# Performance work log

Measured on AMD Instinct MI355X. Metric: run time of the kernel, lower is better.

The kernel has to match this reference:

```python
import jax, jax.numpy as jnp
import numpy as np

B, N, F_IN, S, F_OUT = 16, 128, 8, 8, 64
KN_HID = 32  # kernel_network=[32]
FC_HID = 32


def setup_inputs() -> dict:
    key = jax.random.key(0)
    ks = jax.random.split(key, 13)
    # sparse-ish binary adjacency (batch mode, dense storage)
    A = (jax.random.uniform(ks[0], (B, N, N)) < 0.1).astype(jnp.float32)
    X = jax.random.normal(ks[1], (B, N, F_IN), jnp.float32)
    E = jax.random.normal(ks[2], (B, N, N, S), jnp.float32)
    sc = 0.1
    return {
        "A": A, "X": X, "E": E,
        # ECCConv edge-kernel network: Dense(32, relu) -> Dense(F_IN*F_OUT, linear)
        "kn_w1": jax.random.normal(ks[3], (S, KN_HID), jnp.float32) * sc,
        "kn_b1": jnp.zeros((KN_HID,), jnp.float32),
        "kn_w2": jax.random.normal(ks[4], (KN_HID, F_IN * F_OUT), jnp.float32) * sc,
        "kn_b2": jnp.zeros((F_IN * F_OUT,), jnp.float32),
        # ECCConv root weight + bias
        "root_w": jax.random.normal(ks[5], (F_IN, F_OUT), jnp.float32) * sc,
        "conv_b": jnp.zeros((F_OUT,), jnp.float32),
        # Dense(32, relu)
        "fc_w": jax.random.normal(ks[6], (F_OUT, FC_HID), jnp.float32) * sc,
        "fc_b": jnp.zeros((FC_HID,), jnp.float32),
        # Dense(1, sigmoid)
        "out_w": jax.random.normal(ks[7], (FC_HID, 1), jnp.float32) * sc,
        "out_b": jnp.zeros((1,), jnp.float32),
    }


def reference(A, X, E, kn_w1, kn_b1, kn_w2, kn_b2, root_w, conv_b,
              fc_w, fc_b, out_w, out_b):
    # --- ECCConv (Spektral, batch mode) ---
    # edge-conditioned kernel network: per edge-pair MLP
    h = jax.nn.relu(E @ kn_w1 + kn_b1)            # [B,N,N,32]
    kernel = h @ kn_w2 + kn_b2                    # [B,N,N,F_in*F_out]
    kernel = kernel.reshape(A.shape[0], A.shape[1], A.shape[2], X.shape[-1], root_w.shape[-1])
    kernel = kernel * A[..., None, None]          # mask by adjacency
    # out[b,n,o] = sum_{i,f} kernel[b,n,i,f,o] * X[b,i,f]
    out = jnp.einsum("bnifo,bif->bno", kernel, X)
    out = out + X @ root_w + conv_b               # root weight + bias
    x = jax.nn.relu(out)                          # [B,N,F_out]
    # --- GlobalAvgPool over nodes ---
    x = x.mean(axis=1)                            # [B,F_out]
    # --- Dense head ---
    x = jax.nn.relu(x @ fc_w + fc_b)              # [B,32]
    return jax.nn.sigmoid(x @ out_w + out_b)      # [B,1]
```

## Files before the change

### kernel.cpp

```cpp
#include <hip/hip_runtime.h>
#include <math.h>

#define B_    16
#define N_    128
#define F_IN_ 8
#define S_    8
#define F_OUT_ 64
#define KN_HID_ 32
#define FC_HID_ 32

#define NODE_OFF  0

__global__ __launch_bounds__(256) void k2_fused(
    const float* __restrict__ A, const float* __restrict__ X,
    const float* __restrict__ E,
    const float* __restrict__ kn_w1, const float* __restrict__ kn_b1,
    const float* __restrict__ kn_w2, const float* __restrict__ kn_b2,
    const float* __restrict__ root_w, const float* __restrict__ conv_b,
    float* __restrict__ ws)
{
    __shared__ float Xlds[N_ * F_IN_];
    __shared__ float Elds[4][2][N_ * S_];
    __shared__ float Tlds[4][2][264];

    const int t    = threadIdx.x;
    const int lane = t & 63;
    const int wave = t >> 6;
    const int h2   = lane >> 5;
    const int j    = lane & 31;
    const int b    = blockIdx.x >> 4;
    const int bn0  = blockIdx.x * 8 + wave * 2;

    const float4* __restrict__ Xg4 = (const float4*)(X + b * N_ * F_IN_);
    ((float4*)Xlds)[t] = Xg4[t];

    float w1j[S_];
#pragma unroll
    for (int s = 0; s < S_; ++s) w1j[s] = kn_w1[s * KN_HID_ + j];
    const float b1j = kn_b1[j];

    float4 e4[2][4];
    float a0[2], a1[2];
#pragma unroll
    for (int nn = 0; nn < 2; ++nn) {
        const int bn = bn0 + nn;
        const float4* __restrict__ Eg4 = (const float4*)(E + (size_t)bn * N_ * S_);
#pragma unroll
        for (int q = 0; q < 4; ++q) e4[nn][q] = Eg4[q * 64 + lane];
        a0[nn] = A[(size_t)bn * N_ + lane];
        a1[nn] = A[(size_t)bn * N_ + 64 + lane];
    }
#pragma unroll
    for (int nn = 0; nn < 2; ++nn) {
        float4* __restrict__ El4 = (float4*)Elds[wave][nn];
#pragma unroll
        for (int q = 0; q < 4; ++q) El4[q * 64 + lane] = e4[nn][q];
    }
    __syncthreads();

    const float4* __restrict__ Xl4 = (const float4*)Xlds;

#pragma unroll
    for (int nn = 0; nn < 2; ++nn) {
        const unsigned long long m0 = __ballot(a0[nn] != 0.f);
        const unsigned long long m1 = __ballot(a1[nn] != 0.f);
        const float* __restrict__ Eln = Elds[wave][nn];

        float T[4] = {0.f, 0.f, 0.f, 0.f};
        float xs[4] = {0.f, 0.f, 0.f, 0.f};

#pragma unroll
        for (int half = 0; half < 2; ++half) {
            unsigned long long m = half ? m1 : m0;
            while (m) {
                const int i = __builtin_ctzll(m) + half * 64;
                m &= m - 1;

                const float ev = Eln[i * S_ + (lane & 7)];
                float hv = b1j;
#pragma unroll
                for (int s = 0; s < S_; ++s)
                    hv += __shfl(ev, s) * w1j[s];
                hv = hv > 0.f ? hv : 0.f;

                const float4 xf = Xl4[i * 2 + h2];
                T[0] += hv * xf.x;  T[1] += hv * xf.y;
                T[2] += hv * xf.z;  T[3] += hv * xf.w;
                xs[0] += xf.x; xs[1] += xf.y; xs[2] += xf.z; xs[3] += xf.w;
            }
        }

        float4* __restrict__ Tl4 = (float4*)Tlds[wave][nn];
        Tl4[j * 2 + h2] = make_float4(T[0], T[1], T[2], T[3]);
        if (j == 0)
            Tl4[64 + h2] = make_float4(xs[0], xs[1], xs[2], xs[3]);
    }

    const float* __restrict__ T0 = Tlds[wave][0];
    const float* __restrict__ T1 = Tlds[wave][1];
    float acc0 = 0.f, acc1 = 0.f;
#pragma unroll 8
    for (int kf = 0; kf < 256; ++kf) {
        const float w = kn_w2[kf * F_OUT_ + lane];
        acc0 += T0[kf] * w;
        acc1 += T1[kf] * w;
    }
#pragma unroll
    for (int f = 0; f < F_IN_; ++f) {
        const float w = kn_b2[f * F_OUT_ + lane];
        acc0 += T0[256 + f] * w;
        acc1 += T1[256 + f] * w;
    }

    const float cb = conv_b[lane];
#pragma unroll
    for (int nn = 0; nn < 2; ++nn) {
        const int bn = bn0 + nn;
        const int n  = bn & (N_ - 1);
        float r = (nn == 0) ? acc0 : acc1;
#pragma unroll
        for (int f = 0; f < F_IN_; ++f)
            r += Xlds[n * F_IN_ + f] * root_w[f * F_OUT_ + lane];
        r += cb;
        r = r > 0.f ? r : 0.f;
        ws[NODE_OFF + (size_t)bn * F_OUT_ + lane] = r;
    }
}

__global__ __launch_bounds__(256) void k3_head(
    const float* __restrict__ fc_w, const float* __restrict__ fc_b,
    const float* __restrict__ out_w, const float* __restrict__ out_b,
    const float* __restrict__ ws, float* __restrict__ out)
{
    const int b = blockIdx.x;
    const int t = threadIdx.x;
    const int o = t & 63;
    const int g = t >> 6;

    float p = 0.f;
    for (int n = g; n < N_; n += 4)
        p += ws[NODE_OFF + (size_t)(b * N_ + n) * F_OUT_ + o];

    __shared__ float red[4][F_OUT_];
    __shared__ float pm[F_OUT_];
    __shared__ float y[FC_HID_];
    red[g][o] = p;
    __syncthreads();

    if (t < F_OUT_)
        pm[t] = (red[0][t] + red[1][t] + red[2][t] + red[3][t]) * (1.0f / (float)N_);
    __syncthreads();

    if (t < FC_HID_) {
        float v = fc_b[t];
#pragma unroll
        for (int o2 = 0; o2 < F_OUT_; ++o2) v += pm[o2] * fc_w[o2 * FC_HID_ + t];
        y[t] = v > 0.f ? v : 0.f;
    }
    __syncthreads();

    if (t == 0) {
        float z = out_b[0];
#pragma unroll
        for (int q = 0; q < FC_HID_; ++q) z += y[q] * out_w[q];
        out[b] = 1.f / (1.f + expf(-z));
    }
}

extern "C" void kernel_launch(void* const* d_in, const int* in_sizes, int n_in,
                              void* d_out, int out_size, void* d_ws, size_t ws_size,
                              hipStream_t stream)
{
    const float* A      = (const float*)d_in[0];
    const float* X      = (const float*)d_in[1];
    const float* E      = (const float*)d_in[2];
    const float* kn_w1  = (const float*)d_in[3];
    const float* kn_b1  = (const float*)d_in[4];
    const float* kn_w2  = (const float*)d_in[5];
    const float* kn_b2  = (const float*)d_in[6];
    const float* root_w = (const float*)d_in[7];
    const float* conv_b = (const float*)d_in[8];
    const float* fc_w   = (const float*)d_in[9];
    const float* fc_b   = (const float*)d_in[10];
    const float* out_w  = (const float*)d_in[11];
    const float* out_b  = (const float*)d_in[12];

    float* ws  = (float*)d_ws;
    float* out = (float*)d_out;

    k2_fused<<<B_ * N_ / 8, 256, 0, stream>>>(A, X, E, kn_w1, kn_b1,
                                              kn_w2, kn_b2, root_w, conv_b, ws);
    k3_head<<<B_, 256, 0, stream>>>(fc_w, fc_b, out_w, out_b, ws, out);
}
```

Before: 106.5 us.

## Gather E only for adjacent edges and vectorize the kn_w2 contraction

Drops the bulk staging of each node's full E rows into LDS and instead reads E straight from global memory for nonzero adjacency entries only, prefetching the next edge's values one step ahead. Because about a tenth of the edges are present, this is meant to cut E traffic and LDS use, at the cost of scattered, latency-bound loads. The kn_w2/kn_b2 contraction is also restructured so each lane loads float4 weights over a quarter of the K range, followed by a cross-lane shuffle reduction. The root-weight epilogue and the output stores are vectorized the same way.

New measurement: 107.8 us. No clear change (+1.3%).

```diff
diff --git a/kernel.cpp b/kernel.cpp
--- a/kernel.cpp
+++ b/kernel.cpp
@@ -20,7 +20,6 @@
     float* __restrict__ ws)
 {
     __shared__ float Xlds[N_ * F_IN_];
-    __shared__ float Elds[4][2][N_ * S_];
     __shared__ float Tlds[4][2][264];
 
     const int t    = threadIdx.x;
@@ -31,52 +30,48 @@
     const int b    = blockIdx.x >> 4;
     const int bn0  = blockIdx.x * 8 + wave * 2;
 
-    const float4* __restrict__ Xg4 = (const float4*)(X + b * N_ * F_IN_);
-    ((float4*)Xlds)[t] = Xg4[t];
+    ((float4*)Xlds)[t] = ((const float4*)(X + b * N_ * F_IN_))[t];
 
     float w1j[S_];
 #pragma unroll
     for (int s = 0; s < S_; ++s) w1j[s] = kn_w1[s * KN_HID_ + j];
     const float b1j = kn_b1[j];
 
-    float4 e4[2][4];
     float a0[2], a1[2];
 #pragma unroll
     for (int nn = 0; nn < 2; ++nn) {
         const int bn = bn0 + nn;
-        const float4* __restrict__ Eg4 = (const float4*)(E + (size_t)bn * N_ * S_);
-#pragma unroll
-        for (int q = 0; q < 4; ++q) e4[nn][q] = Eg4[q * 64 + lane];
         a0[nn] = A[(size_t)bn * N_ + lane];
         a1[nn] = A[(size_t)bn * N_ + 64 + lane];
     }
+    __syncthreads();
+
+    const float4* __restrict__ Xl4 = (const float4*)Xlds;
+
 #pragma unroll
     for (int nn = 0; nn < 2; ++nn) {
-        float4* __restrict__ El4 = (float4*)Elds[wave][nn];
-#pragma unroll
-        for (int q = 0; q < 4; ++q) El4[q * 64 + lane] = e4[nn][q];
-    }
-    __syncthreads();
-
-    const float4* __restrict__ Xl4 = (const float4*)Xlds;
-
-#pragma unroll
-    for (int nn = 0; nn < 2; ++nn) {
-        const unsigned long long m0 = __ballot(a0[nn] != 0.f);
-        const unsigned long long m1 = __ballot(a1[nn] != 0.f);
-        const float* __restrict__ Eln = Elds[wave][nn];
-
-        float T[4] = {0.f, 0.f, 0.f, 0.f};
+        const int bn = bn0 + nn;
+        const unsigned long long mA = __ballot(a0[nn] != 0.f);
+        const unsigned long long mB = __ballot(a1[nn] != 0.f);
+        const float* __restrict__ Eb = E + (size_t)bn * N_ * S_ + (lane & 7);
+
+        float T[4]  = {0.f, 0.f, 0.f, 0.f};
         float xs[4] = {0.f, 0.f, 0.f, 0.f};
 
 #pragma unroll
         for (int half = 0; half < 2; ++half) {
-            unsigned long long m = half ? m1 : m0;
-            while (m) {
-                const int i = __builtin_ctzll(m) + half * 64;
-                m &= m - 1;
-
-                const float ev = Eln[i * S_ + (lane & 7)];
+            unsigned long long m = half ? mB : mA;
+            if (!m) continue;
+            int i = __builtin_ctzll(m) + half * 64;
+            m &= m - 1;
+            float ev = Eb[i * S_];
+            while (true) {
+                int inext = -1; float evnext = 0.f;
+                if (m) {
+                    inext = __builtin_ctzll(m) + half * 64;
+                    m &= m - 1;
+                    evnext = Eb[inext * S_];
+                }
                 float hv = b1j;
 #pragma unroll
                 for (int s = 0; s < S_; ++s)
@@ -87,6 +82,9 @@
                 T[0] += hv * xf.x;  T[1] += hv * xf.y;
                 T[2] += hv * xf.z;  T[3] += hv * xf.w;
                 xs[0] += xf.x; xs[1] += xf.y; xs[2] += xf.z; xs[3] += xf.w;
+
+                if (inext < 0) break;
+                i = inext; ev = evnext;
             }
         }
 
@@ -96,34 +94,56 @@
             Tl4[64 + h2] = make_float4(xs[0], xs[1], xs[2], xs[3]);
     }
 
+    const int q = lane & 15;
+    const int g = lane >> 4;
     const float* __restrict__ T0 = Tlds[wave][0];
     const float* __restrict__ T1 = Tlds[wave][1];
-    float acc0 = 0.f, acc1 = 0.f;
+    const float4* __restrict__ W4 = (const float4*)kn_w2;
+    const float4* __restrict__ B4 = (const float4*)kn_b2;
+
+    float4 acc0 = make_float4(0.f, 0.f, 0.f, 0.f);
+    float4 acc1 = make_float4(0.f, 0.f, 0.f, 0.f);
 #pragma unroll 8
-    for (int kf = 0; kf < 256; ++kf) {
-        const float w = kn_w2[kf * F_OUT_ + lane];
-        acc0 += T0[kf] * w;
-        acc1 += T1[kf] * w;
-    }
-#pragma unroll
-    for (int f = 0; f < F_IN_; ++f) {
-        const float w = kn_b2[f * F_OUT_ + lane];
-        acc0 += T0[256 + f] * w;
-        acc1 += T1[256 + f] * w;
-    }
-
-    const float cb = conv_b[lane];
+    for (int kf = g; kf < 256; kf += 4) {
+        const float4 w = W4[kf * 16 + q];
+        const float t0 = T0[kf], t1 = T1[kf];
+        acc0.x += t0 * w.x; acc0.y += t0 * w.y; acc0.z += t0 * w.z; acc0.w += t0 * w.w;
+        acc1.x += t1 * w.x; acc1.y += t1 * w.y; acc1.z += t1 * w.z; acc1.w += t1 * w.w;
+    }
+#pragma unroll
+    for (int f = g; f < F_IN_; f += 4) {
+        const float4 w = B4[f * 16 + q];
+        const float t0 = T0[256 + f], t1 = T1[256 + f];
+        acc0.x += t0 * w.x; acc0.y += t0 * w.y; acc0.z += t0 * w.z; acc0.w += t0 * w.w;
+        acc1.x += t1 * w.x; acc1.y += t1 * w.y; acc1.z += t1 * w.z; acc1.w += t1 * w.w;
+    }
+
+#pragma unroll
+    for (int d = 16; d < 64; d <<= 1) {
+        acc0.x += __shfl_xor(acc0.x, d); acc0.y += __shfl_xor(acc0.y, d);
+        acc0.z += __shfl_xor(acc0.z, d); acc0.w += __shfl_xor(acc0.w, d);
+        acc1.x += __shfl_xor(acc1.x, d); acc1.y += __shfl_xor(acc1.y, d);
+        acc1.z += __shfl_xor(acc1.z, d); acc1.w += __shfl_xor(acc1.w, d);
+    }
+
+    const float4* __restrict__ R4 = (const float4*)root_w;
+    const float4 cb = ((const float4*)conv_b)[q];
 #pragma unroll
     for (int nn = 0; nn < 2; ++nn) {
         const int bn = bn0 + nn;
         const int n  = bn & (N_ - 1);
-        float r = (nn == 0) ? acc0 : acc1;
-#pragma unroll
-        for (int f = 0; f < F_IN_; ++f)
-            r += Xlds[n * F_IN_ + f] * root_w[f * F_OUT_ + lane];
-        r += cb;
-        r = r > 0.f ? r : 0.f;
-        ws[NODE_OFF + (size_t)bn * F_OUT_ + lane] = r;
+        float4 r = (nn == 0) ? acc0 : acc1;
+        r.x += cb.x; r.y += cb.y; r.z += cb.z; r.w += cb.w;
+#pragma unroll
+        for (int f = 0; f < F_IN_; ++f) {
+            const float xv = Xlds[n * F_IN_ + f];
+            const float4 rw = R4[f * 16 + q];
+            r.x += xv * rw.x; r.y += xv * rw.y; r.z += xv * rw.z; r.w += xv * rw.w;
+        }
+        r.x = r.x > 0.f ? r.x : 0.f;  r.y = r.y > 0.f ? r.y : 0.f;
+        r.z = r.z > 0.f ? r.z : 0.f;  r.w = r.w > 0.f ? r.w : 0.f;
+        if (g == 0)
+            ((float4*)(ws + NODE_OFF + (size_t)bn * F_OUT_))[q] = r;
     }
 }
 
@@ -162,7 +182,7 @@
     if (t == 0) {
         float z = out_b[0];
 #pragma unroll
-        for (int q = 0; q < FC_HID_; ++q) z += y[q] * out_w[q];
+        for (int qq = 0; qq < FC_HID_; ++qq) z += y[qq] * out_w[qq];
         out[b] = 1.f / (1.f + expf(-z));
     }
 }
```
